# Performance work log

Hardware: AMD Instinct MI355X
Metric: run time of the kernel (lower is better)

The kernel has to match this reference:

```python
import jax, jax.numpy as jnp
import numpy as np

EPS = 1e-12  # torch F.normalize eps

def _cam(fmap, w):
    # torch: sum over C of w[1,C,R,1,1] * fmap[B,C,1,H,W] -> (B,R,H,W)
    # expressed as an efficient contraction (1x1 conv / GEMM)
    return jnp.einsum('bchw,rc->brhw', fmap, w)

def _embedding(fmap, w, b):
    pooled = fmap.mean(axis=(-2, -1))           # (B,C) AdaptiveAvgPool2d(1)
    return pooled @ w.T + b                      # (B,R)

def _certainty(cam):
    B, R = cam.shape[:2]
    flat = cam.reshape(B, R, -1)
    return jnp.std(flat, axis=-1, ddof=1)        # torch .std() is unbiased

def _avgpool_to(x, out_hw):
    # adaptive avg pool with integer ratio == reshape-mean
    B, R, H, W = x.shape
    oh, ow = out_hw
    return x.reshape(B, R, oh, H // oh, ow, W // ow).mean(axis=(3, 5))

def _link(low_cam, high_cam):
    low_cam = jax.lax.stop_gradient(low_cam)
    high_cam = jax.lax.stop_gradient(high_cam)
    if low_cam.shape[2:] != high_cam.shape[2:]:
        low_cam = _avgpool_to(low_cam, high_cam.shape[2:])
    B = low_cam.shape[0]
    lo = low_cam.reshape(B, low_cam.shape[1], -1)
    hi = high_cam.reshape(B, high_cam.shape[1], -1)
    lo = lo / jnp.maximum(jnp.linalg.norm(lo, axis=-1, keepdims=True), EPS)
    hi = hi / jnp.maximum(jnp.linalg.norm(hi, axis=-1, keepdims=True), EPS)
    return jnp.einsum('bmi,bni->mn', lo, hi) / B

def setup_inputs() -> dict:
    key = jax.random.key(0)
    ks = jax.random.split(key, 6)
    B, R = 64, 128
    chans = [512, 1024, 2048]
    hws = [28, 14, 7]
    inp = {}
    for l in range(3):
        inp[f'fmap{l}'] = jax.random.normal(ks[l], (B, chans[l], hws[l], hws[l]), dtype=jnp.float32)
        inp[f'w{l}'] = jax.random.normal(ks[3 + l], (R, chans[l]), dtype=jnp.float32) * 0.02
        inp[f'b{l}'] = jnp.zeros((R,), dtype=jnp.float32)
    return inp

def reference(fmap0, fmap1, fmap2, w0, b0, w1, b1, w2, b2):
    fmaps = [fmap0, fmap1, fmap2]
    ws = [w0, w1, w2]
    bs = [b0, b1, b2]
    embeddings = [_embedding(f, w, b) for f, w, b in zip(fmaps, ws, bs)]
    cams = [_cam(f, w) for f, w in zip(fmaps, ws)]
    certainties = [_certainty(c) for c in cams]
    links = [_link(cams[l - 1], cams[l]) for l in range(1, 3)]
    return (*embeddings, *certainties, *links)
```

## Files before the change

### kernel.cpp

```cpp
#include <hip/hip_runtime.h>
#include <stdint.h>

#define R 128
#define NB 64

#define CAM0_OFF 0
#define CAM1_OFF 6422528
#define CAM2_OFF 8028160
#define POOL0_OFF 8429568
#define POOL1_OFF 10035200
#define WB_OFF    10436608
#define PART_OFF  10665984
#define NORM_OFF  12763136

typedef __bf16 bf16;
typedef bf16 v2bf __attribute__((ext_vector_type(2)));
typedef bf16 v8bf __attribute__((ext_vector_type(8)));
typedef float f4v __attribute__((ext_vector_type(4)));

#define ASM_BARRIER() asm volatile("s_waitcnt lgkmcnt(0)\n\ts_barrier" ::: "memory")

__global__ void prep_w(const float* __restrict__ w0, const float* __restrict__ w1,
                       const float* __restrict__ w2, bf16* __restrict__ wb) {
    int id = blockIdx.x * 256 + threadIdx.x;
    float v;
    if (id < 65536)       v = w0[id];
    else if (id < 196608) v = w1[id - 65536];
    else                  v = w2[id - 196608];
    wb[id] = (bf16)v;
}

__global__ __launch_bounds__(512) void cam_gemm(
    const float* __restrict__ f0, const float* __restrict__ f1,
    const float* __restrict__ f2, const bf16* __restrict__ wb,
    float* __restrict__ ws) {
    __shared__ bf16 ldsB[2][64 * 72];

    int bid = blockIdx.x, tid = threadIdx.x;
    int lvl, b, i0;
    if (bid < 64)       { lvl = 2; b = bid; i0 = 0; }
    else if (bid < 320) { int t = bid - 64; lvl = 1; b = t >> 2;
                          int ti = t & 3; i0 = ti < 3 ? ti * 64 : 132; }
    else                { int t = bid - 320; lvl = 0; b = t / 13;
                          int ti = t - b * 13; i0 = ti < 12 ? ti * 64 : 720; }
    const int C  = (lvl == 0) ? 512 : (lvl == 1) ? 1024 : 2048;
    const int HW = (lvl == 0) ? 784 : (lvl == 1) ? 196  : 49;
    const float* fmap = (lvl == 0) ? f0 : (lvl == 1) ? f1 : f2;
    const bf16*  wbl  = wb + ((lvl == 0) ? 0 : (lvl == 1) ? 65536 : 196608);
    float* cam = ws + ((lvl == 0) ? CAM0_OFF : (lvl == 1) ? CAM1_OFF : CAM2_OFF);

    int d = tid >> 4;
    int ku2 = d * 2;
    int i4 = (tid & 15) * 4;
    int gbase = b * C * HW + ku2 * HW + i0 + i4;
    int ldsd[4];
    int i4c[4];
#pragma unroll
    for (int e = 0; e < 4; ++e) {
        int i = i4 + e;
        int grp = (d >> 2) ^ ((i >> 3) & 7);
        ldsd[e] = i * 72 + grp * 8 + (d & 3) * 2;
        i4c[e] = min(i, 48);
    }
    const int lane = tid & 63, wave = tid >> 6;
    const int lm = lane & 15, q = lane >> 4;
    const int wm = (wave >> 1) * 32, wn = (wave & 1) * 32;
    int irow[2], ixor[2];
#pragma unroll
    for (int sn = 0; sn < 2; ++sn) {
        irow[sn] = wn + sn * 16 + lm;
        ixor[sn] = (irow[sn] >> 3) & 7;
    }
    const bf16* arow[2];
#pragma unroll
    for (int sm = 0; sm < 2; ++sm)
        arow[sm] = wbl + (wm + sm * 16 + lm) * C + q * 8;

    auto loadT = [&](int kc, float4 (&r)[2]) {
        if (HW != 49) {
            const float* p = fmap + gbase + kc * HW;
            r[0] = *(const float4*)p;
            r[1] = *(const float4*)(p + HW);
        } else {
            const float* p = fmap + b * C * 49 + (kc + ku2) * 49;
            r[0].x = p[i4c[0]]; r[0].y = p[i4c[1]];
            r[0].z = p[i4c[2]]; r[0].w = p[i4c[3]];
            r[1].x = p[49 + i4c[0]]; r[1].y = p[49 + i4c[1]];
            r[1].z = p[49 + i4c[2]]; r[1].w = p[49 + i4c[3]];
        }
    };
    auto stage = [&](float4 (&r)[2], bf16* buf) {
        v2bf t0 = { (bf16)r[0].x, (bf16)r[1].x };
        v2bf t1 = { (bf16)r[0].y, (bf16)r[1].y };
        v2bf t2 = { (bf16)r[0].z, (bf16)r[1].z };
        v2bf t3 = { (bf16)r[0].w, (bf16)r[1].w };
        *(v2bf*)&buf[ldsd[0]] = t0;
        *(v2bf*)&buf[ldsd[1]] = t1;
        *(v2bf*)&buf[ldsd[2]] = t2;
        *(v2bf*)&buf[ldsd[3]] = t3;
    };

    f4v acc[2][2] = {};
    auto comp = [&](int kc, const bf16* buf) {
#pragma unroll
        for (int ks = 0; ks < 64; ks += 32) {
            v8bf af[2];
#pragma unroll
            for (int sm = 0; sm < 2; ++sm)
                af[sm] = *(const v8bf*)(arow[sm] + kc + ks);
            v8bf bfr[2];
#pragma unroll
            for (int sn = 0; sn < 2; ++sn) {
                int grp = (q + ((ks >> 5) << 2)) ^ ixor[sn];
                bfr[sn] = *(const v8bf*)&buf[irow[sn] * 72 + grp * 8];
            }
#pragma unroll
            for (int sm = 0; sm < 2; ++sm)
#pragma unroll
                for (int sn = 0; sn < 2; ++sn)
                    acc[sm][sn] = __builtin_amdgcn_mfma_f32_16x16x32_bf16(
                        af[sm], bfr[sn], acc[sm][sn], 0, 0, 0);
        }
    };

    const int nIter = C >> 6;
    float4 rA[2], rB[2];
    loadT(0, rA);
    loadT(64, rB);
    for (int t = 0; t < nIter; t += 2) {
        stage(rA, ldsB[0]);
        ASM_BARRIER();
        if (t + 2 < nIter) loadT((t + 2) << 6, rA);
        comp(t << 6, ldsB[0]);
        stage(rB, ldsB[1]);
        ASM_BARRIER();
        if (t + 3 < nIter) loadT((t + 3) << 6, rB);
        comp((t + 1) << 6, ldsB[1]);
    }
#pragma unroll
    for (int sn = 0; sn < 2; ++sn) {
        int i_n = i0 + irow[sn];
        if (i_n < HW) {
            int base = (b * R) * HW + i_n;
#pragma unroll
            for (int sm = 0; sm < 2; ++sm) {
#pragma unroll
                for (int reg = 0; reg < 4; ++reg) {
                    int r = wm + sm * 16 + q * 4 + reg;
                    cam[base + r * HW] = acc[sm][sn][reg];
                }
            }
        }
    }
}

__global__ __launch_bounds__(256) void post_k(
    float* __restrict__ ws, const float* __restrict__ b0,
    const float* __restrict__ b1, const float* __restrict__ b2,
    float* __restrict__ out) {
    __shared__ float plds[4 * 784];
    int gw = blockIdx.x * 4 + (threadIdx.x >> 6);
    int lane = threadIdx.x & 63;
    float* myl = plds + (threadIdx.x >> 6) * 784;
    int lvl = gw >> 13, row = gw & 8191;
    const int HW = (lvl == 0) ? 784 : (lvl == 1) ? 196 : 49;
    const float* cam = ws + ((lvl == 0) ? CAM0_OFF : (lvl == 1) ? CAM1_OFF : CAM2_OFF)
                        + (long)row * HW;
    float s = 0.f, ss = 0.f;
    for (int j = lane; j < HW; j += 64) {
        float v = cam[j]; s += v; ss += v * v; myl[j] = v;
    }
#pragma unroll
    for (int o = 32; o; o >>= 1) { s += __shfl_xor(s, o); ss += __shfl_xor(ss, o); }
    if (lane == 0) {
        const float* bias = (lvl == 0) ? b0 : (lvl == 1) ? b1 : b2;
        float mean = s / (float)HW;
        out[lvl * 8192 + row] = mean + bias[row & 127];
        float var = fmaxf(ss - s * mean, 0.f) / (float)(HW - 1);
        out[24576 + lvl * 8192 + row] = sqrtf(var);
        if (lvl >= 1)
            ws[NORM_OFF + (lvl - 1) * 8192 + row] = 1.0f / fmaxf(sqrtf(ss), 1e-12f);
    }
    if (lvl <= 1) {
        const int OP = (lvl == 0) ? 196 : 49;
        const int OW = (lvl == 0) ? 14 : 7;
        const int IW = (lvl == 0) ? 28 : 14;
        float vals[4]; float ssp = 0.f; int cnt = 0;
        for (int p = lane; p < OP; p += 64) {
            int oh = p / OW, ow = p - oh * OW;
            int i0 = oh * 2 * IW + ow * 2;
            float v = (myl[i0] + myl[i0 + 1] + myl[i0 + IW] + myl[i0 + IW + 1]) * 0.25f;
            vals[cnt++] = v; ssp += v * v;
        }
#pragma unroll
        for (int o = 32; o; o >>= 1) ssp += __shfl_xor(ssp, o);
        float inv = 1.0f / fmaxf(sqrtf(ssp), 1e-12f);
        float* dst = ws + ((lvl == 0) ? POOL0_OFF : POOL1_OFF) + (long)row * OP;
        cnt = 0;
        for (int p = lane; p < OP; p += 64) dst[p] = vals[cnt++] * inv;
    }
}

__device__ inline v8bf load_frag8(const float* __restrict__ row, int k0, int K) {
    v8bf f;
    if (k0 + 8 <= K && (K & 3) == 0) {
        float4 a = *(const float4*)(row + k0);
        float4 c = *(const float4*)(row + k0 + 4);
        f[0] = (bf16)a.x; f[1] = (bf16)a.y; f[2] = (bf16)a.z; f[3] = (bf16)a.w;
        f[4] = (bf16)c.x; f[5] = (bf16)c.y; f[6] = (bf16)c.z; f[7] = (bf16)c.w;
    } else {
#pragma unroll
        for (int j = 0; j < 8; ++j)
            f[j] = (k0 + j < K) ? (bf16)row[k0 + j] : (bf16)0.f;
    }
    return f;
}

__global__ __launch_bounds__(256) void link_mfma_k(const float* __restrict__ ws,
                                                   float* __restrict__ part) {
    int bid = blockIdx.x, tid = threadIdx.x;
    int lk = bid >> 7, rem = bid & 127;
    int b = rem >> 1, mh = rem & 1;
    const int K = lk ? 49 : 196;
    const float* lo = ws + (lk ? POOL1_OFF : POOL0_OFF) + (long)(b * 128 + mh * 64) * K;
    const float* hi = ws + (lk ? CAM2_OFF : CAM1_OFF) + (long)b * 128 * K;
    const float* nrmp = ws + NORM_OFF + lk * 8192 + b * 128;
    int lane = tid & 63, wv = tid >> 6;
    int lm = lane & 15, q = lane >> 4;
    int wm = (wv >> 1) * 32, wn = (wv & 1) * 64;
    f4v acc[2][4] = {};
    for (int kc = 0; kc < K; kc += 32) {
        v8bf af[2], bff[4];
#pragma unroll
        for (int sm = 0; sm < 2; ++sm)
            af[sm] = load_frag8(lo + (long)(wm + sm * 16 + lm) * K, kc + q * 8, K);
#pragma unroll
        for (int sn = 0; sn < 4; ++sn)
            bff[sn] = load_frag8(hi + (long)(wn + sn * 16 + lm) * K, kc + q * 8, K);
#pragma unroll
        for (int sm = 0; sm < 2; ++sm)
#pragma unroll
            for (int sn = 0; sn < 4; ++sn)
                acc[sm][sn] = __builtin_amdgcn_mfma_f32_16x16x32_bf16(
                    af[sm], bff[sn], acc[sm][sn], 0, 0, 0);
    }
#pragma unroll
    for (int sn = 0; sn < 4; ++sn) {
        int n = wn + sn * 16 + lm;
        float sh = nrmp[n];
#pragma unroll
        for (int sm = 0; sm < 2; ++sm) {
#pragma unroll
            for (int reg = 0; reg < 4; ++reg) {
                int m = mh * 64 + wm + sm * 16 + q * 4 + reg;
                part[(long)(lk * 16384 + m * 128 + n) * 64 + b] = acc[sm][sn][reg] * sh;
            }
        }
    }
}

__global__ void linkred_k(const float* __restrict__ part, float* __restrict__ out) {
    int id = blockIdx.x * 256 + threadIdx.x;
    const float* p = part + (long)id * 64;
    float s = 0.f;
#pragma unroll
    for (int j = 0; j < 16; ++j) {
        float4 v = *(const float4*)(p + j * 4);
        s += v.x + v.y + v.z + v.w;
    }
    out[49152 + id] = s * (1.0f / 64.0f);
}

extern "C" void kernel_launch(void* const* d_in, const int* in_sizes, int n_in,
                              void* d_out, int out_size, void* d_ws, size_t ws_size,
                              hipStream_t stream) {
    const float* f0 = (const float*)d_in[0];
    const float* w0 = (const float*)d_in[1];
    const float* b0 = (const float*)d_in[2];
    const float* f1 = (const float*)d_in[3];
    const float* w1 = (const float*)d_in[4];
    const float* b1 = (const float*)d_in[5];
    const float* f2 = (const float*)d_in[6];
    const float* w2 = (const float*)d_in[7];
    const float* b2 = (const float*)d_in[8];
    float* ws = (float*)d_ws;
    float* out = (float*)d_out;
    bf16* wb = (bf16*)(ws + WB_OFF);

    prep_w<<<1792, 256, 0, stream>>>(w0, w1, w2, wb);
    cam_gemm<<<1152, 512, 0, stream>>>(f0, f1, f2, wb, ws);
    post_k<<<6144, 256, 0, stream>>>(ws, b0, b1, b2, out);
    link_mfma_k<<<256, 256, 0, stream>>>(ws, ws + PART_OFF);
    linkred_k<<<128, 256, 0, stream>>>(ws + PART_OFF, out);
}
```

Measured before the change: 309.0 us.

## Deepen CAM GEMM register prefetch and transpose link partials to batch-major layout

The CAM GEMM main loop now prefetches four K-tiles into registers instead of two, alternating between two LDS buffers, so more global loads are in flight ahead of the compute. The link partial buffer changes from batch-innermost to batch-outermost layout, which makes the GEMM epilogue writes contiguous across lanes instead of strided by 64 floats. The reduction kernel now reads with coalesced strided-by-batch accesses. The deeper prefetch costs extra registers and assumes the iteration count is a multiple of four.

```diff
diff --git a/kernel.cpp b/kernel.cpp
--- a/kernel.cpp
+++ b/kernel.cpp
@@ -124,18 +124,16 @@
     };
 
     const int nIter = C >> 6;
-    float4 rA[2], rB[2];
-    loadT(0, rA);
-    loadT(64, rB);
-    for (int t = 0; t < nIter; t += 2) {
-        stage(rA, ldsB[0]);
-        ASM_BARRIER();
-        if (t + 2 < nIter) loadT((t + 2) << 6, rA);
-        comp(t << 6, ldsB[0]);
-        stage(rB, ldsB[1]);
-        ASM_BARRIER();
-        if (t + 3 < nIter) loadT((t + 3) << 6, rB);
-        comp((t + 1) << 6, ldsB[1]);
+    float4 rT[4][2];
+    loadT(0, rT[0]); loadT(64, rT[1]); loadT(128, rT[2]); loadT(192, rT[3]);
+    for (int t = 0; t < nIter; t += 4) {
+#pragma unroll
+        for (int u = 0; u < 4; ++u) {
+            stage(rT[u], ldsB[u & 1]);
+            ASM_BARRIER();
+            if (t + u + 4 < nIter) loadT((t + u + 4) << 6, rT[u]);
+            comp((t + u) << 6, ldsB[u & 1]);
+        }
     }
 #pragma unroll
     for (int sn = 0; sn < 2; ++sn) {
@@ -244,6 +242,7 @@
                 acc[sm][sn] = __builtin_amdgcn_mfma_f32_16x16x32_bf16(
                     af[sm], bff[sn], acc[sm][sn], 0, 0, 0);
     }
+    float* pb = part + (long)b * 32768 + lk * 16384;
 #pragma unroll
     for (int sn = 0; sn < 4; ++sn) {
         int n = wn + sn * 16 + lm;
@@ -253,7 +252,7 @@
 #pragma unroll
             for (int reg = 0; reg < 4; ++reg) {
                 int m = mh * 64 + wm + sm * 16 + q * 4 + reg;
-                part[(long)(lk * 16384 + m * 128 + n) * 64 + b] = acc[sm][sn][reg] * sh;
+                pb[m * 128 + n] = acc[sm][sn][reg] * sh;
             }
         }
     }
@@ -261,14 +260,15 @@
 
 __global__ void linkred_k(const float* __restrict__ part, float* __restrict__ out) {
     int id = blockIdx.x * 256 + threadIdx.x;
-    const float* p = part + (long)id * 64;
-    float s = 0.f;
-#pragma unroll
-    for (int j = 0; j < 16; ++j) {
-        float4 v = *(const float4*)(p + j * 4);
-        s += v.x + v.y + v.z + v.w;
-    }
-    out[49152 + id] = s * (1.0f / 64.0f);
+    float s0 = 0.f, s1 = 0.f, s2 = 0.f, s3 = 0.f;
+#pragma unroll
+    for (int b = 0; b < 64; b += 4) {
+        s0 += part[(long)(b + 0) * 32768 + id];
+        s1 += part[(long)(b + 1) * 32768 + id];
+        s2 += part[(long)(b + 2) * 32768 + id];
+        s3 += part[(long)(b + 3) * 32768 + id];
+    }
+    out[49152 + id] = (s0 + s1 + s2 + s3) * (1.0f / 64.0f);
 }
 
 extern "C" void kernel_launch(void* const* d_in, const int* in_sizes, int n_in,
```

Result: faster. 296.6 us (-4.0%).
